# Performance work log

Measured on AMD Instinct MI355X. Metric: run time of the kernel, lower is better.

Reference implementation:

```python
import jax, jax.numpy as jnp
import numpy as np
import itertools

DIM = 7
N_H2, N_H3 = 21, 77

def _perm_sign(p):
    inv = sum(1 for i in range(len(p)) for j in range(i + 1, len(p)) if p[i] > p[j])
    return -1.0 if inv % 2 else 1.0

def _build_wedge_constants():
    # C[a,b,c] = sign of (pair_a, pair_b, triple_c) as a permutation of (0..6),
    # zero unless the 2+2+3 indices are disjoint (coefficient of the volume form
    # in omega_a ^ omega_b ^ Phi_c on ordered-multi-index components).
    idx2 = list(itertools.combinations(range(DIM), 2))   # 21 ordered pairs
    idx3 = list(itertools.combinations(range(DIM), 3))   # 35 ordered triples
    C = np.zeros((len(idx2), len(idx2), len(idx3)), dtype=np.float32)
    for a, pa in enumerate(idx2):
        sa = set(pa)
        for b, pb in enumerate(idx2):
            if sa & set(pb):
                continue
            sab = sa | set(pb)
            for c, pc in enumerate(idx3):
                full = pa + pb + pc
                if sab.isdisjoint(pc):
                    C[a, b, c] = _perm_sign(full)
    return jnp.asarray(C)

C_WEDGE = _build_wedge_constants()  # (21, 21, 35), sparse structure constants

def setup_inputs() -> dict:
    key = jax.random.key(0)
    k1, k2, k3 = jax.random.split(key, 3)
    batch = 4096
    omega = jax.random.normal(k1, (batch, N_H2, 21), dtype=jnp.float32)
    Phi = jax.random.normal(k2, (batch, N_H3, 35), dtype=jnp.float32)
    metric = jax.random.normal(k3, (batch, DIM, DIM), dtype=jnp.float32)
    return {"omega": omega, "Phi": Phi, "metric": metric}

def reference(omega, Phi, metric):
    # Monte-Carlo volume weights, normalized (normalize=True path)
    vol = jnp.sqrt(jnp.abs(jnp.linalg.det(metric)))        # (n,)
    w = vol / vol.sum()
    # Fused triple wedge contraction replacing the 21*21*77 python loops:
    # D[n,i,j,c] = sum_{a,b} C[a,b,c] omega[n,i,a] omega[n,j,b]
    D = jnp.einsum('abc,nia,njb->nijc', C_WEDGE, omega, omega)
    Pw = Phi * w[:, None, None]                             # fold MC weight into Phi
    S = jnp.einsum('nijc,nkc->ijk', D, Pw)                  # (21,21,77), symmetric in i,j
    # Original code writes +integral for j>=i and forces -integral for j<i
    upper = jnp.triu(jnp.ones((N_H2, N_H2), dtype=bool))[:, :, None]
    Y = jnp.where(upper, S, -S)
    # Gram matrix and spectrum
    M = jnp.einsum('ijk,ijl->kl', Y, Y)                     # (77,77)
    eigenvalues = jnp.linalg.eigvalsh(M)[::-1]              # descending, like torch path
    return Y, M, eigenvalues
```

## Files before the change

kernel.cpp:

```cpp
#include <hip/hip_runtime.h>
#include <math.h>

#define NBATCH 4096
#define NH2 21
#define NK 77
#define NC 35
#define NIJ 441
#define Y_SIZE 33957
#define M_SIZE 5929
#define VOLOFF Y_SIZE
#define VSUM (Y_SIZE + 4096)
#define NPAIR 231
#define BLK 512
#define NPB 8
#define GRID_B (NBATCH / NPB)
#define EIGT 640

#define NSLOT 16
#define SLOT_STRIDE 17792
#define WS2OFF (NSLOT * SLOT_STRIDE)

#define SZ_OMEGA  (NBATCH * NH2 * NH2)
#define SZ_PHI    (NBATCH * NK * NC)
#define SZ_METRIC (NBATCH * 7 * 7)

struct WTab {
  int a[NC][6];
  int b[NC][6];
  int sg[NC][6];
};

constexpr WTab make_wtab() {
  WTab W{};
  int p0[21] = {}, p1[21] = {};
  int idx = 0;
  for (int x = 0; x < 7; ++x)
    for (int y = x + 1; y < 7; ++y) { p0[idx] = x; p1[idx] = y; ++idx; }
  int t0[35] = {}, t1[35] = {}, t2[35] = {};
  idx = 0;
  for (int x = 0; x < 7; ++x)
    for (int y = x + 1; y < 7; ++y)
      for (int z = y + 1; z < 7; ++z) { t0[idx] = x; t1[idx] = y; t2[idx] = z; ++idx; }
  int cnt[35] = {};
  for (int a = 0; a < 21; ++a)
    for (int b = 0; b < 21; ++b) {
      int pa0 = p0[a], pa1 = p1[a], pb0 = p0[b], pb1 = p1[b];
      if (pa0 == pb0 || pa0 == pb1 || pa1 == pb0 || pa1 == pb1) continue;
      bool used[7] = {};
      used[pa0] = true; used[pa1] = true; used[pb0] = true; used[pb1] = true;
      int tr[3] = {}; int k = 0;
      for (int x = 0; x < 7; ++x) if (!used[x]) tr[k++] = x;
      int c = -1;
      for (int cc = 0; cc < 35; ++cc)
        if (t0[cc] == tr[0] && t1[cc] == tr[1] && t2[cc] == tr[2]) { c = cc; break; }
      int perm[7] = {pa0, pa1, pb0, pb1, tr[0], tr[1], tr[2]};
      int inv = 0;
      for (int i = 0; i < 7; ++i)
        for (int j = i + 1; j < 7; ++j)
          if (perm[i] > perm[j]) ++inv;
      W.a[c][cnt[c]] = a; W.b[c][cnt[c]] = b; W.sg[c][cnt[c]] = (inv & 1) ? -1 : 1;
      ++cnt[c];
    }
  return W;
}

__device__ __forceinline__ int trioff(int i) { return 21 * i - (i * (i - 1)) / 2; }

__device__ __forceinline__ unsigned f2bf(float x) {
  union { float f; unsigned u; } v; v.f = x;
  return ((v.u + 0x7FFFu + ((v.u >> 16) & 1u)) >> 16) & 0xFFFFu;
}

typedef float f32x4 __attribute__((ext_vector_type(4)));
typedef float f32x2 __attribute__((ext_vector_type(2)));
typedef short s16x8 __attribute__((ext_vector_type(8)));

__device__ __forceinline__ f32x2 pk_fma(f32x2 a, f32x2 b, f32x2 c) {
  f32x2 d;
  asm volatile("v_pk_fma_f32 %0, %1, %2, %3" : "=v"(d) : "v"(a), "v"(b), "v"(c));
  return d;
}

template <int CTRL>
__device__ __forceinline__ float dppadd(float x) {
  union { float f; int i; } u, r;
  u.f = x;
  r.i = __builtin_amdgcn_update_dpp(0, u.i, CTRL, 0xF, 0xF, true);
  return x + r.f;
}
__device__ __forceinline__ float oct_sum(float x) {
  x = dppadd<0xB1>(x);
  x = dppadd<0x4E>(x);
  x = dppadd<0x141>(x);
  return x;
}
__device__ __forceinline__ float wave_sum(float x) {
  x = dppadd<0xB1>(x);
  x = dppadd<0x4E>(x);
  x = dppadd<0x141>(x);
  x = dppadd<0x140>(x);
  x = dppadd<0x142>(x);
  x = dppadd<0x143>(x);
  return x;
}
__device__ __forceinline__ float readlane63(float x) {
  union { float f; int i; } u; u.f = x;
  union { int i; float f; } r;
  r.i = __builtin_amdgcn_readlane(u.i, 63);
  return r.f;
}

__global__ __launch_bounds__(256) void vol_kernel(const float* __restrict__ metric,
                                                  float* __restrict__ out) {
  const int n = blockIdx.x * 256 + threadIdx.x;
  double a[7][7];
#pragma unroll
  for (int r = 0; r < 7; ++r)
#pragma unroll
    for (int c = 0; c < 7; ++c) a[r][c] = (double)metric[n * 49 + r * 7 + c];

  double det = 1.0;
#pragma unroll
  for (int k = 0; k < 7; ++k) {
#pragma unroll
    for (int r = k + 1; r < 7; ++r) {
      bool sw = fabs(a[r][k]) > fabs(a[k][k]);
#pragma unroll
      for (int c = k; c < 7; ++c) {
        double u = a[k][c], v = a[r][c];
        a[k][c] = sw ? v : u;
        a[r][c] = sw ? u : v;
      }
    }
    det *= a[k][k];
    double inv = (a[k][k] != 0.0) ? 1.0 / a[k][k] : 0.0;
#pragma unroll
    for (int r = k + 1; r < 7; ++r) {
      double f = a[r][k] * inv;
#pragma unroll
      for (int c = k + 1; c < 7; ++c) a[r][c] -= f * a[k][c];
    }
  }
  float vol = (float)sqrt(fabs(det));
  out[VOLOFF + n] = vol;

  float s = vol;
#pragma unroll
  for (int off = 32; off > 0; off >>= 1) s += __shfl_down(s, off, 64);
  __shared__ float partial[4];
  const int lane = threadIdx.x & 63, wv = threadIdx.x >> 6;
  if (lane == 0) partial[wv] = s;
  __syncthreads();
  if (threadIdx.x == 0)
    atomicAdd(out + VSUM, partial[0] + partial[1] + partial[2] + partial[3]);
}

__global__ __launch_bounds__(BLK) void contract_kernel(const float* __restrict__ omega,
                                                       const float* __restrict__ Phi,
                                                       const float* __restrict__ out,
                                                       float* __restrict__ wsS) {
  constexpr WTab W = make_wtab();
  __shared__ __align__(16) short ldsD[256 * 80];
  __shared__ __align__(16) short ldsP[80 * 80];
  __shared__ __align__(16) float ldsO[NH2 * 28];

  const int t = threadIdx.x;
  const int lane = t & 63;
  const int wv = t >> 6;
  const int quad = lane >> 4;
  const int col = lane & 15;
  const int n0 = blockIdx.x * NPB;

  for (int f = t; f < 256 * 40; f += BLK) ((int*)ldsD)[f] = 0;
  for (int f = t; f < 80 * 40; f += BLK) ((int*)ldsP)[f] = 0;

  const bool roleA = (t < NPAIR);
  const bool roleB = (t >= 256) && (t < 256 + NPAIR);
  int pi = 0, pj = 0;
  {
    const int p = roleA ? t : (roleB ? (t - 256) : 0);
    int i = 0;
    while (i < 20 && trioff(i + 1) <= p) ++i;
    pi = i;
    pj = p - trioff(i) + i;
  }

  float rA = 0.0f, rB[6], rvn;
  {
    const float* om = omega + n0 * 441;
    const float* ph = Phi + n0 * 2695;
    if (t < 441) rA = om[t];
#pragma unroll
    for (int j = 0; j < 6; ++j) {
      const int e = t + j * BLK;
      rB[j] = (e < 2695) ? ph[e] : 0.0f;
    }
    rvn = out[VOLOFF + n0];
  }

  f32x4 acc[2][5];
#pragma unroll
  for (int mi = 0; mi < 2; ++mi)
#pragma unroll
    for (int nt = 0; nt < 5; ++nt) acc[mi][nt] = (f32x4){0.f, 0.f, 0.f, 0.f};

  for (int it = 0; it < NPB; ++it) {
    __syncthreads();

    if (t < 441) ldsO[(t / 21) * 28 + (t % 21)] = rA;
    {
      const float vn = rvn;
#pragma unroll
      for (int j = 0; j < 6; ++j) {
        const int e = t + j * BLK;
        if (e < 2695) {
          const int q = e / 35, c = e % 35;
          ldsP[q * 80 + c] = (short)f2bf(vn * rB[j]);
        }
      }
    }
    __syncthreads();

    if (it + 1 < NPB) {
      const int n1 = n0 + it + 1;
      const float* om2 = omega + n1 * 441;
      const float* ph2 = Phi + n1 * 2695;
      if (t < 441) rA = om2[t];
#pragma unroll
      for (int j = 0; j < 6; ++j) {
        const int e = t + j * BLK;
        if (e < 2695) rB[j] = ph2[e];
      }
      rvn = out[VOLOFF + n1];
    }

    if (roleA || roleB) {
      float wi[21], wj[21];
      const float* oi = ldsO + pi * 28;
      const float* oj = ldsO + pj * 28;
#pragma unroll
      for (int a = 0; a < 20; a += 4) {
        float4 v = *(const float4*)(oi + a);
        wi[a] = v.x; wi[a + 1] = v.y; wi[a + 2] = v.z; wi[a + 3] = v.w;
        float4 u = *(const float4*)(oj + a);
        wj[a] = u.x; wj[a + 1] = u.y; wj[a + 2] = u.z; wj[a + 3] = u.w;
      }
      wi[20] = oi[20]; wj[20] = oj[20];

      if (roleA) {
        float d[18];
#pragma unroll
        for (int c = 0; c < 18; ++c) {
          float dd = 0.0f;
#pragma unroll
          for (int u = 0; u < 6; ++u)
            dd = fmaf((W.sg[c][u] > 0) ? wi[W.a[c][u]] : -wi[W.a[c][u]], wj[W.b[c][u]], dd);
          d[c] = dd;
        }
        int* Drow = (int*)ldsD + t * 40;
#pragma unroll
        for (int k2 = 0; k2 < 9; ++k2)
          Drow[k2] = (int)(f2bf(d[2 * k2]) | (f2bf(d[2 * k2 + 1]) << 16));
      } else {
        float d[17];
#pragma unroll
        for (int c = 18; c < 35; ++c) {
          float dd = 0.0f;
#pragma unroll
          for (int u = 0; u < 6; ++u)
            dd = fmaf((W.sg[c][u] > 0) ? wi[W.a[c][u]] : -wi[W.a[c][u]], wj[W.b[c][u]], dd);
          d[c - 18] = dd;
        }
        int* Drow = (int*)ldsD + (t - 256) * 40;
#pragma unroll
        for (int k2 = 0; k2 < 8; ++k2)
          Drow[9 + k2] = (int)(f2bf(d[2 * k2]) | (f2bf(d[2 * k2 + 1]) << 16));
        Drow[17] = (int)f2bf(d[16]);
      }
    }
    __syncthreads();

#pragma unroll
    for (int s = 0; s < 2; ++s) {
      const int kof = s * 32 + quad * 8;
      s16x8 a0 = *(const s16x8*)(ldsD + ((wv * 2 + 0) * 16 + col) * 80 + kof);
      s16x8 a1 = *(const s16x8*)(ldsD + ((wv * 2 + 1) * 16 + col) * 80 + kof);
      s16x8 b[5];
#pragma unroll
      for (int nt = 0; nt < 5; ++nt)
        b[nt] = *(const s16x8*)(ldsP + (nt * 16 + col) * 80 + kof);
#pragma unroll
      for (int nt = 0; nt < 5; ++nt) {
        acc[0][nt] = __builtin_amdgcn_mfma_f32_16x16x32_bf16(a0, b[nt], acc[0][nt], 0, 0, 0);
        acc[1][nt] = __builtin_amdgcn_mfma_f32_16x16x32_bf16(a1, b[nt], acc[1][nt], 0, 0, 0);
      }
    }
  }

  float* slot = wsS + (size_t)(blockIdx.x & (NSLOT - 1)) * SLOT_STRIDE;
#pragma unroll
  for (int mi = 0; mi < 2; ++mi) {
    const int mt = wv * 2 + mi;
#pragma unroll
    for (int r = 0; r < 4; ++r) {
      const int m = mt * 16 + quad * 4 + r;
      if (m < NPAIR) {
#pragma unroll
        for (int nt = 0; nt < 5; ++nt) {
          const int q = nt * 16 + col;
          if (q < 77) atomicAdd(&slot[m * NK + q], acc[mi][nt][r]);
        }
      }
    }
  }
}

__global__ __launch_bounds__(256) void finalize_y(const float* __restrict__ wsS,
                                                  float* __restrict__ out) {
  const int e = blockIdx.x * 256 + threadIdx.x;
  if (e >= NPAIR * NK) return;
  const int p = e / NK, k = e % NK;
  int i = 0;
  while (i < 20 && trioff(i + 1) <= p) ++i;
  const int j = p - trioff(i) + i;
  float v = 0.0f;
#pragma unroll
  for (int s = 0; s < NSLOT; ++s) v += wsS[(size_t)s * SLOT_STRIDE + p * NK + k];
  v *= 1.0f / out[VSUM];
  out[(i * 21 + j) * NK + k] = v;
  if (j != i) out[(j * 21 + i) * NK + k] = -v;
}

__global__ __launch_bounds__(EIGT) void gram_kernel(const float* __restrict__ Y,
                                                    float* __restrict__ Mout) {
  const int k = blockIdx.x;
  const int t = threadIdx.x;
  const int l = t >> 3, s = t & 7;
  float acc = 0.0f;
  if (l < NK) {
    for (int ij = s; ij < NIJ; ij += 8)
      acc = fmaf(Y[ij * NK + k], Y[ij * NK + l], acc);
  }
  acc = oct_sum(acc);
  if (s == 0 && l < NK) Mout[k * NK + l] = acc;
}

__global__ __launch_bounds__(64, 1) void tridiag_kernel(const float* __restrict__ Min,
                                                        float* __restrict__ ws2) {
  const int l = threadIdx.x;
  const int br = l >> 3, bc = l & 7;
  f32x2 A2[10][5];
#pragma unroll
  for (int r = 0; r < 10; ++r) {
    const int g = 10 * br + r;
#pragma unroll
    for (int c2 = 0; c2 < 5; ++c2) {
      const int gc0 = 10 * bc + 2 * c2;
      A2[r][c2][0] = (g < 77 && gc0 < 77) ? Min[g * 77 + gc0] : 0.0f;
      A2[r][c2][1] = (g < 77 && gc0 + 1 < 77) ? Min[g * 77 + gc0 + 1] : 0.0f;
    }
  }

#pragma unroll 1
  for (int kb = 0; kb < 8; ++kb) {
    const int idx_c = kb * 8 + bc;
#pragma unroll
    for (int ko = 0; ko < 10; ++ko) {
      if (kb == 7 && ko >= 5) break;
      const int k = kb * 10 + ko;

      f32x2 rowk2[5];
#pragma unroll
      for (int c2 = 0; c2 < 5; ++c2) {
        rowk2[c2][0] = __shfl(A2[ko][c2][0], idx_c, 64);
        rowk2[c2][1] = __shfl(A2[ko][c2][1], idx_c, 64);
      }

      float part = 0.0f, xpart = 0.0f;
      if (br == 0) {
#pragma unroll
        for (int c2 = 0; c2 < 5; ++c2) {
          const int gc0 = 10 * bc + 2 * c2;
          const float x0 = rowk2[c2][0], x1v = rowk2[c2][1];
          part += (gc0 > k) ? x0 * x0 : 0.0f;
          part += (gc0 + 1 > k) ? x1v * x1v : 0.0f;
          xpart += (gc0 == k + 1) ? x0 : 0.0f;
          xpart += (gc0 + 1 == k + 1) ? x1v : 0.0f;
        }
      }
      part = wave_sum(part);
      xpart = wave_sum(xpart);
      const float sigma2 = readlane63(part);
      if (sigma2 < 1e-26f) {
        if (l == 0) ws2[80 + k] = 0.0f;
        continue;
      }
      const float x1 = readlane63(xpart);
      const float sigma = sqrtf(sigma2);
      const float alpha = (x1 >= 0.0f) ? -sigma : sigma;
      const float beta = 1.0f / (sigma2 - alpha * x1);
      const float xha = x1 - alpha;
      if (l == 0) ws2[80 + k] = alpha;

      f32x2 vc2[5];
#pragma unroll
      for (int c2 = 0; c2 < 5; ++c2) {
        const int gc0 = 10 * bc + 2 * c2;
        vc2[c2][0] = (gc0 > k) ? ((gc0 == k + 1) ? xha : rowk2[c2][0]) : 0.0f;
        vc2[c2][1] = (gc0 + 1 > k) ? ((gc0 + 1 == k + 1) ? xha : rowk2[c2][1]) : 0.0f;
      }
      float vr[10];
#pragma unroll
      for (int c2 = 0; c2 < 5; ++c2) {
        vr[2 * c2] = __shfl(vc2[c2][0], br, 64);
        vr[2 * c2 + 1] = __shfl(vc2[c2][1], br, 64);
      }

      float p[10];
#pragma unroll
      for (int r = 0; r < 10; ++r) {
        f32x2 a = (f32x2){0.f, 0.f};
#pragma unroll
        for (int c2 = 0; c2 < 5; ++c2) a = pk_fma(A2[r][c2], vc2[c2], a);
        p[r] = a[0] + a[1];
      }
#pragma unroll
      for (int r = 0; r < 10; ++r) {
        p[r] = oct_sum(p[r]) * beta;
        p[r] = (10 * br + r > k) ? p[r] : 0.0f;
      }

      float kp = 0.0f;
      if (bc == 0) {
#pragma unroll
        for (int r = 0; r < 10; ++r) kp = fmaf(p[r], vr[r], kp);
      }
      kp = wave_sum(kp);
      const float hb = 0.5f * beta * readlane63(kp);

      float w[10];
#pragma unroll
      for (int r = 0; r < 10; ++r) w[r] = fmaf(-hb, vr[r], p[r]);
      const int diag = 9 * bc;
      f32x2 wc2[5];
#pragma unroll
      for (int c2 = 0; c2 < 5; ++c2) {
        wc2[c2][0] = __shfl(w[2 * c2], diag, 64);
        wc2[c2][1] = __shfl(w[2 * c2 + 1], diag, 64);
      }

#pragma unroll
      for (int r = 0; r < 10; ++r) {
        const f32x2 nv = (f32x2){-vr[r], -vr[r]};
        const f32x2 nw = (f32x2){-w[r], -w[r]};
#pragma unroll
        for (int c2 = 0; c2 < 5; ++c2)
          A2[r][c2] = pk_fma(nv, wc2[c2], pk_fma(nw, vc2[c2], A2[r][c2]));
      }
    }
  }

  if (br == bc) {
#pragma unroll
    for (int e = 0; e < 10; ++e)
      ws2[10 * br + e] = (e & 1) ? A2[e][e / 2][1] : A2[e][e / 2][0];
  }
  if (l == 63) ws2[80 + 75] = A2[6][2][1];
}

__global__ __launch_bounds__(EIGT) void bisect_kernel(const float* __restrict__ ws2,
                                                      float* __restrict__ eout) {
  __shared__ float dsh[80], esh[80], e2sh[80];
  __shared__ float red[10], red2[10];
  const int t = threadIdx.x;
  const int lane = t & 63, wv = t >> 6;
  if (t < 80) {
    dsh[t] = ws2[t];
    esh[t] = (t < 76) ? ws2[80 + t] : 0.0f;
  }
  __syncthreads();
  if (t < 76) e2sh[t] = esh[t] * esh[t];

  float lo_ = 1e30f, hi_ = -1e30f;
  if (t < 77) {
    const float r = ((t > 0) ? fabsf(esh[t - 1]) : 0.0f) +
                    ((t < 76) ? fabsf(esh[t]) : 0.0f);
    lo_ = dsh[t] - r;
    hi_ = dsh[t] + r;
  }
#pragma unroll
  for (int off = 1; off < 64; off <<= 1) {
    lo_ = fminf(lo_, __shfl_xor(lo_, off, 64));
    hi_ = fmaxf(hi_, __shfl_xor(hi_, off, 64));
  }
  if (lane == 0) { red[wv] = lo_; red2[wv] = hi_; }
  __syncthreads();
  lo_ = red[0]; hi_ = red2[0];
#pragma unroll
  for (int u = 1; u < 10; ++u) { lo_ = fminf(lo_, red[u]); hi_ = fmaxf(hi_, red2[u]); }
  const float span = hi_ - lo_;
  const float glo = lo_ - 0.001f * span - 1e-6f;
  const float ghi = hi_ + 0.001f * span + 1e-6f;

  {
    const int e = t >> 3;
    const int s = t & 7;
    const int g = (t & 63) >> 3;
    float lo = glo, hi = ghi;
    for (int r = 0; r < 13; ++r) {
      const float step = (hi - lo) * (1.0f / 9.0f);
      const float x = fmaf(step, (float)(s + 1), lo);
      float q = dsh[0] - x;
      int cnt = (q < 0.0f);
#pragma unroll 4
      for (int i = 1; i < 77; ++i) {
        q = (fabsf(q) < 1e-30f) ? -1e-30f : q;
        q = dsh[i] - x - e2sh[i - 1] * __builtin_amdgcn_rcpf(q);
        cnt += (q < 0.0f);
      }
      const unsigned long long mask = __ballot(cnt > e);
      const int b = (int)((mask >> (g * 8)) & 0xFFull);
      const int z = b ? __builtin_ctz(b) : 8;
      const float nlo = fmaf(step, (float)z, lo);
      hi = (z == 8) ? hi : fmaf(step, (float)(z + 1), lo);
      lo = nlo;
    }
    if (s == 0 && e < 77) eout[76 - e] = 0.5f * (lo + hi);
  }
}

extern "C" void kernel_launch(void* const* d_in, const int* in_sizes, int n_in,
                              void* d_out, int out_size, void* d_ws, size_t ws_size,
                              hipStream_t stream) {
  const float* omega  = (const float*)d_in[0];
  const float* Phi    = (const float*)d_in[1];
  const float* metric = (const float*)d_in[2];
  for (int q = 0; q < n_in && q < 3; ++q) {
    if (in_sizes[q] == SZ_OMEGA)       omega  = (const float*)d_in[q];
    else if (in_sizes[q] == SZ_PHI)    Phi    = (const float*)d_in[q];
    else if (in_sizes[q] == SZ_METRIC) metric = (const float*)d_in[q];
  }

  float* out = (float*)d_out;
  float* ws  = (float*)d_ws;

  hipMemsetAsync(d_out, 0, (size_t)out_size * sizeof(float), stream);
  hipMemsetAsync(d_ws, 0, (size_t)WS2OFF * sizeof(float), stream);

  hipLaunchKernelGGL(vol_kernel, dim3(NBATCH / 256), dim3(256), 0, stream, metric, out);
  hipLaunchKernelGGL(contract_kernel, dim3(GRID_B), dim3(BLK), 0, stream,
                     omega, Phi, out, ws);
  hipLaunchKernelGGL(finalize_y, dim3((NPAIR * NK + 255) / 256), dim3(256), 0, stream,
                     ws, out);
  hipLaunchKernelGGL(gram_kernel, dim3(NK), dim3(EIGT), 0, stream,
                     out, out + Y_SIZE);
  hipLaunchKernelGGL(tridiag_kernel, dim3(1), dim3(64), 0, stream,
                     out + Y_SIZE, ws + WS2OFF);
  hipLaunchKernelGGL(bisect_kernel, dim3(1), dim3(EIGT), 0, stream,
                     ws + WS2OFF, out + Y_SIZE + M_SIZE);
}
```

Baseline: 348.9 us.

## Prefetch next Householder row via early rank-2 update and overlap shuffles

In the single-wave tridiagonalization loop, the row needed by the next Householder step is updated first. It is then broadcast with shuffles (both column and row views) before the rest of the rank-2 update runs, so the shuffle latency overlaps with the remaining FMAs. The row-view vector vr is now built from the prefetched row instead of a separate shuffle of vc2. The transposed w vector is rebuilt from a shuffled p plus a packed FMA rather than shuffled directly. This adds register pressure (rc/rr arrays) and extra shuffles per step to shorten the serial dependency chain of each iteration.

```diff
diff --git a/kernel.cpp b/kernel.cpp
--- a/kernel.cpp
+++ b/kernel.cpp
@@ -361,27 +361,31 @@
     }
   }
 
+  float rc[10], rr[10];
+#pragma unroll
+  for (int c2 = 0; c2 < 5; ++c2) {
+    rc[2 * c2]     = __shfl(A2[0][c2][0], bc, 64);
+    rc[2 * c2 + 1] = __shfl(A2[0][c2][1], bc, 64);
+    rr[2 * c2]     = __shfl(A2[0][c2][0], br, 64);
+    rr[2 * c2 + 1] = __shfl(A2[0][c2][1], br, 64);
+  }
+
 #pragma unroll 1
   for (int kb = 0; kb < 8; ++kb) {
-    const int idx_c = kb * 8 + bc;
 #pragma unroll
     for (int ko = 0; ko < 10; ++ko) {
       if (kb == 7 && ko >= 5) break;
       const int k = kb * 10 + ko;
-
-      f32x2 rowk2[5];
-#pragma unroll
-      for (int c2 = 0; c2 < 5; ++c2) {
-        rowk2[c2][0] = __shfl(A2[ko][c2][0], idx_c, 64);
-        rowk2[c2][1] = __shfl(A2[ko][c2][1], idx_c, 64);
-      }
+      const int nko = (ko + 1) % 10;
+      const int nkb = kb + (ko == 9 ? 1 : 0);
+      const int nic = nkb * 8 + bc, nir = nkb * 8 + br;
 
       float part = 0.0f, xpart = 0.0f;
       if (br == 0) {
 #pragma unroll
         for (int c2 = 0; c2 < 5; ++c2) {
           const int gc0 = 10 * bc + 2 * c2;
-          const float x0 = rowk2[c2][0], x1v = rowk2[c2][1];
+          const float x0 = rc[2 * c2], x1v = rc[2 * c2 + 1];
           part += (gc0 > k) ? x0 * x0 : 0.0f;
           part += (gc0 + 1 > k) ? x1v * x1v : 0.0f;
           xpart += (gc0 == k + 1) ? x0 : 0.0f;
@@ -393,6 +397,13 @@
       const float sigma2 = readlane63(part);
       if (sigma2 < 1e-26f) {
         if (l == 0) ws2[80 + k] = 0.0f;
+#pragma unroll
+        for (int c2 = 0; c2 < 5; ++c2) {
+          rc[2 * c2]     = __shfl(A2[nko][c2][0], nic, 64);
+          rc[2 * c2 + 1] = __shfl(A2[nko][c2][1], nic, 64);
+          rr[2 * c2]     = __shfl(A2[nko][c2][0], nir, 64);
+          rr[2 * c2 + 1] = __shfl(A2[nko][c2][1], nir, 64);
+        }
         continue;
       }
       const float x1 = readlane63(xpart);
@@ -403,17 +414,15 @@
       if (l == 0) ws2[80 + k] = alpha;
 
       f32x2 vc2[5];
+      float vr[10];
 #pragma unroll
       for (int c2 = 0; c2 < 5; ++c2) {
         const int gc0 = 10 * bc + 2 * c2;
-        vc2[c2][0] = (gc0 > k) ? ((gc0 == k + 1) ? xha : rowk2[c2][0]) : 0.0f;
-        vc2[c2][1] = (gc0 + 1 > k) ? ((gc0 + 1 == k + 1) ? xha : rowk2[c2][1]) : 0.0f;
-      }
-      float vr[10];
-#pragma unroll
-      for (int c2 = 0; c2 < 5; ++c2) {
-        vr[2 * c2] = __shfl(vc2[c2][0], br, 64);
-        vr[2 * c2 + 1] = __shfl(vc2[c2][1], br, 64);
+        vc2[c2][0] = (gc0 > k) ? ((gc0 == k + 1) ? xha : rc[2 * c2]) : 0.0f;
+        vc2[c2][1] = (gc0 + 1 > k) ? ((gc0 + 1 == k + 1) ? xha : rc[2 * c2 + 1]) : 0.0f;
+        const int gr0 = 10 * br + 2 * c2;
+        vr[2 * c2] = (gr0 > k) ? ((gr0 == k + 1) ? xha : rr[2 * c2]) : 0.0f;
+        vr[2 * c2 + 1] = (gr0 + 1 > k) ? ((gr0 + 1 == k + 1) ? xha : rr[2 * c2 + 1]) : 0.0f;
       }
 
       float p[10];
@@ -430,6 +439,13 @@
         p[r] = (10 * br + r > k) ? p[r] : 0.0f;
       }
 
+      f32x2 pc2[5];
+#pragma unroll
+      for (int c2 = 0; c2 < 5; ++c2) {
+        pc2[c2][0] = __shfl(p[2 * c2], 9 * bc, 64);
+        pc2[c2][1] = __shfl(p[2 * c2 + 1], 9 * bc, 64);
+      }
+
       float kp = 0.0f;
       if (bc == 0) {
 #pragma unroll
@@ -441,16 +457,28 @@
       float w[10];
 #pragma unroll
       for (int r = 0; r < 10; ++r) w[r] = fmaf(-hb, vr[r], p[r]);
-      const int diag = 9 * bc;
+      const f32x2 mhb = (f32x2){-hb, -hb};
       f32x2 wc2[5];
 #pragma unroll
+      for (int c2 = 0; c2 < 5; ++c2) wc2[c2] = pk_fma(mhb, vc2[c2], pc2[c2]);
+
+      {
+        const f32x2 nv = (f32x2){-vr[nko], -vr[nko]};
+        const f32x2 nw = (f32x2){-w[nko], -w[nko]};
+#pragma unroll
+        for (int c2 = 0; c2 < 5; ++c2)
+          A2[nko][c2] = pk_fma(nv, wc2[c2], pk_fma(nw, vc2[c2], A2[nko][c2]));
+      }
+#pragma unroll
       for (int c2 = 0; c2 < 5; ++c2) {
-        wc2[c2][0] = __shfl(w[2 * c2], diag, 64);
-        wc2[c2][1] = __shfl(w[2 * c2 + 1], diag, 64);
-      }
-
+        rc[2 * c2]     = __shfl(A2[nko][c2][0], nic, 64);
+        rc[2 * c2 + 1] = __shfl(A2[nko][c2][1], nic, 64);
+        rr[2 * c2]     = __shfl(A2[nko][c2][0], nir, 64);
+        rr[2 * c2 + 1] = __shfl(A2[nko][c2][1], nir, 64);
+      }
 #pragma unroll
       for (int r = 0; r < 10; ++r) {
+        if (r == nko) continue;
         const f32x2 nv = (f32x2){-vr[r], -vr[r]};
         const f32x2 nw = (f32x2){-w[r], -w[r]};
 #pragma unroll
```

Measured after the change: 353.7 us. No clear change (+1.4%).
